# Kernel optimization log

Hardware: AMD Instinct MI355X
Metric: run time of the kernel (lower is better)

The kernel has to match this reference:

```python
import jax, jax.numpy as jnp
import numpy as np
from jax import lax

B, C, H, W, K = 64, 64, 128, 128, 4
EPS = 1e-5

def setup_inputs() -> dict:
    key = jax.random.key(0)
    ks = jax.random.split(key, 8)
    def p(i, shape, scale=0.05):
        return jax.random.normal(ks[i], shape, dtype=jnp.float32) * scale
    return {
        "rgb":   jax.random.normal(ks[0], (B, C, H, W), dtype=jnp.float32),
        "depth": jax.random.normal(ks[1], (B, C, H, W), dtype=jnp.float32),
        # kernel_gen MLP: Linear(2C->C), Linear(C -> K*C*9)
        "w1": p(2, (C, 2 * C)), "b1": jnp.zeros((C,), jnp.float32),
        "w2": p(3, (K * C * 9, C)), "b2": jnp.zeros((K * C * 9,), jnp.float32),
        # freq_decompose: Conv3x3(C->C) + BN (eval-mode stats)
        "fd_w": p(4, (C, C, 3, 3)), "fd_b": jnp.zeros((C,), jnp.float32),
        "fd_scale": jnp.ones((C,), jnp.float32), "fd_bias": jnp.zeros((C,), jnp.float32),
        "fd_mean": jnp.zeros((C,), jnp.float32), "fd_var": jnp.ones((C,), jnp.float32),
        # fusion: Conv1x1(2C->C) + BN
        "fu_w": p(5, (C, 2 * C, 1, 1)), "fu_b": jnp.zeros((C,), jnp.float32),
        "fu_scale": jnp.ones((C,), jnp.float32), "fu_bias": jnp.zeros((C,), jnp.float32),
        "fu_mean": jnp.zeros((C,), jnp.float32), "fu_var": jnp.ones((C,), jnp.float32),
    }

def _bn(x, scale, bias, mean, var):
    # eval-mode batchnorm over channel axis 1
    inv = scale / jnp.sqrt(var + EPS)
    return x * inv[None, :, None, None] + (bias - mean * inv)[None, :, None, None]

def _conv(x, w, pad):
    return lax.conv_general_dilated(x, w, (1, 1), ((pad, pad), (pad, pad)),
                                    dimension_numbers=("NCHW", "OIHW", "NCHW"))

def reference(rgb, depth, w1, b1, w2, b2,
              fd_w, fd_b, fd_scale, fd_bias, fd_mean, fd_var,
              fu_w, fu_b, fu_scale, fu_bias, fu_mean, fu_var):
    b, c, h, w = rgb.shape
    k = w2.shape[0] // (c * 9)
    # kernel generation: global avg pool over concat -> MLP
    pooled = jnp.concatenate([rgb, depth], axis=1).mean(axis=(2, 3))  # [B, 2C]
    hid = jax.nn.relu(pooled @ w1.T + b1)                             # [B, C]
    kernels = (hid @ w2.T + b2).reshape(b, k, c, 3, 3)                # [B, K, C, 3, 3]
    norms = jnp.linalg.norm(kernels.reshape(b, k, -1), axis=2)        # [B, K]
    attn = jax.nn.softmax(norms, axis=1)
    weighted_kernel = jnp.einsum("bk,bkcij->bcij", attn, kernels)     # [B, C, 3, 3]
    # NOTE: faithful to the torch code: plain conv2d with out_channels=B (requires B==C)
    dynamic_feat = _conv(rgb, weighted_kernel, 1)                     # [B, B, H, W]
    freq_feat = jax.nn.relu(_bn(_conv(depth, fd_w, 1) + fd_b[None, :, None, None],
                                fd_scale, fd_bias, fd_mean, fd_var))
    cat = jnp.concatenate([dynamic_feat, freq_feat], axis=1)          # [B, 2C, H, W]
    fused = jax.nn.relu(_bn(_conv(cat, fu_w, 0) + fu_b[None, :, None, None],
                            fu_scale, fu_bias, fu_mean, fu_var))
    return fused
```

## Files before the change

kernel.cpp:

```cpp
#include <hip/hip_runtime.h>
#include <hip/hip_bf16.h>

#define CB 64
#define HH 128
#define WW 128
#define KK 4
#define EPSV 1e-5f
#define HWSZ (HH*WW)

using f32x4   = __attribute__((ext_vector_type(4))) float;
using f32x16  = __attribute__((ext_vector_type(16))) float;
using short8  = __attribute__((ext_vector_type(8))) short;

static constexpr size_t WS_POOLED = 0;
static constexpr size_t WS_HID    = 8192;
static constexpr size_t WS_KERN   = 12288;
static constexpr size_t WS_SSQ    = 159744;
static constexpr size_t WS_WK     = 160000;
static constexpr size_t WS_EFFW   = 196864;
static constexpr size_t WS_FUW2   = 233728;
static constexpr size_t WS_FDINV  = 237824;
static constexpr size_t WS_FDBETA = 237888;
static constexpr size_t WS_FUINV  = 237952;
static constexpr size_t WS_FUBETA = 238016;
static constexpr size_t WT3_BYTE = 49152;
static constexpr size_t WFD_BYTE = 49152 + 73728;
static constexpr size_t W1_BYTE  = 49152 + 147456;
static constexpr size_t WS_PART_BYTE   = 4u << 20;
static constexpr size_t WS_DEPTHT_BYTE = 8u << 20;
static constexpr size_t WS_RGBT_BYTE   = 140u << 20;


__global__ void k_consts(const float* __restrict__ fd_scale, const float* __restrict__ fd_bias,
                         const float* __restrict__ fd_mean, const float* __restrict__ fd_var,
                         const float* __restrict__ fd_b,
                         const float* __restrict__ fu_scale, const float* __restrict__ fu_bias,
                         const float* __restrict__ fu_mean, const float* __restrict__ fu_var,
                         const float* __restrict__ fu_b,
                         float* __restrict__ ws) {
    int c = threadIdx.x;
    if (c < CB) {
        float fdi = fd_scale[c] / sqrtf(fd_var[c] + EPSV);
        ws[WS_FDINV + c]  = fdi;
        ws[WS_FDBETA + c] = (fd_b[c] - fd_mean[c]) * fdi + fd_bias[c];
        float fui = fu_scale[c] / sqrtf(fu_var[c] + EPSV);
        ws[WS_FUINV + c]  = fui;
        ws[WS_FUBETA + c] = (fu_b[c] - fu_mean[c]) * fui + fu_bias[c];
    }
}

__device__ __forceinline__ unsigned int pack_bf16(float a, float b) {
    __hip_bfloat16 ha = __float2bfloat16(a), hb = __float2bfloat16(b);
    return (unsigned int)*(unsigned short*)&ha | ((unsigned int)*(unsigned short*)&hb << 16);
}

__global__ __launch_bounds__(256) void k_nhwc(const float* __restrict__ rgb,
                                              const float* __restrict__ depth,
                                              unsigned int* __restrict__ rgbT,
                                              unsigned int* __restrict__ depthT,
                                              float* __restrict__ part) {
    int g = blockIdx.x;
    int b = blockIdx.y;
    int t = threadIdx.x;

    if (g == 64) {
        unsigned int* dR0 = rgbT   + ((size_t)b * 130 + 0)   * 130 * 32;
        unsigned int* dR1 = rgbT   + ((size_t)b * 130 + 129) * 130 * 32;
        unsigned int* dD0 = depthT + ((size_t)b * 130 + 0)   * 130 * 32;
        unsigned int* dD1 = depthT + ((size_t)b * 130 + 129) * 130 * 32;
        for (int i = t; i < 130 * 32; i += 256) {
            dR0[i] = 0u; dR1[i] = 0u; dD0[i] = 0u; dD1[i] = 0u;
        }
        return;
    }
    int y0 = g * 2;
    {
        int tensor = t >> 7, side = (t >> 6) & 1, row = (t >> 5) & 1, j = t & 31;
        unsigned int* d = tensor ? depthT : rgbT;
        d[(((size_t)b * 130 + (y0 + 1 + row)) * 130 + (side ? 129 : 0)) * 32 + j] = 0u;
    }

    __shared__ float staged[32][260];
    __shared__ float poolacc[128];
    int w = t >> 6, lane = t & 63;

    #pragma unroll
    for (int ph = 0; ph < 4; ++ph) {
        const float* src = (ph >> 1) ? depth : rgb;
        int chbase = (ph & 1) * 32;
        if (ph) __syncthreads();
        #pragma unroll
        for (int i = 0; i < 8; ++i) {
            int flat = i * 256 + t;
            int c = flat >> 6, f4 = flat & 63;
            const float4* sp = (const float4*)(src + ((size_t)(b * CB + chbase + c)) * HWSZ
                                               + (size_t)y0 * WW);
            float4 v = sp[f4];
            *(float4*)&staged[c][f4 * 4] = v;
            float s = v.x + v.y + v.z + v.w;
            #pragma unroll
            for (int off = 32; off; off >>= 1) s += __shfl_down(s, off, 64);
            if (lane == 0) poolacc[(ph >> 1) * 64 + chbase + i * 4 + w] = s;
        }
        __syncthreads();
        {
            int row = t >> 7, x = t & 127;
            unsigned int u[16];
            #pragma unroll
            for (int k = 0; k < 16; ++k)
                u[k] = pack_bf16(staged[2 * k][t], staged[2 * k + 1][t]);
            unsigned int* dst = (ph >> 1) ? depthT : rgbT;
            unsigned int* dp = dst + (((size_t)b * 130 + (y0 + 1 + row)) * 130 + 1 + x) * 32
                                   + (chbase >> 1);
            *(uint4*)dp        = *(uint4*)&u[0];
            *(uint4*)(dp + 4)  = *(uint4*)&u[4];
            *(uint4*)(dp + 8)  = *(uint4*)&u[8];
            *(uint4*)(dp + 12) = *(uint4*)&u[12];
        }
    }
    __syncthreads();
    if (t < 128)
        part[((size_t)b * 64 + g) * 128 + t] = poolacc[t];
}

__global__ __launch_bounds__(256) void k_pool2(const float* __restrict__ part,
                                               float* __restrict__ ws) {
    int b = blockIdx.x, t = threadIdx.x, cc = t & 127, q = t >> 7;
    float s = 0.f;
    for (int g = q * 32; g < q * 32 + 32; ++g)
        s += part[((size_t)b * 64 + g) * 128 + cc];
    __shared__ float red[2][128];
    red[q][cc] = s;
    __syncthreads();
    if (t < 128)
        ws[WS_POOLED + b * 128 + t] = (red[0][t] + red[1][t]) * (1.f / 16384.f);
}

__global__ void k_hid(const float* __restrict__ w1, const float* __restrict__ b1,
                      float* __restrict__ ws) {
    __shared__ float p[128];
    int b = blockIdx.x, j = threadIdx.x;
    p[j] = ws[WS_POOLED + b * 128 + j];
    __syncthreads();
    if (j < CB) {
        float s = b1[j];
        const float* wr = w1 + j * 128;
        #pragma unroll 8
        for (int i = 0; i < 128; ++i) s += p[i] * wr[i];
        ws[WS_HID + b * CB + j] = fmaxf(s, 0.f);
    }
}

__global__ __launch_bounds__(256) void k_kern(const float* __restrict__ w2, const float* __restrict__ b2,
                                              float* __restrict__ ws) {
    __shared__ float h[CB];
    int b = blockIdx.x, t = threadIdx.x;
    if (t < CB) h[t] = ws[WS_HID + b * CB + t];
    __syncthreads();
    float local = 0.f;
    #pragma unroll
    for (int r9 = 0; r9 < 9; ++r9) {
        int r = t * 9 + r9;
        float s = b2[r];
        const float* wr = w2 + r * CB;
        #pragma unroll 8
        for (int m = 0; m < CB; ++m) s += h[m] * wr[m];
        ws[WS_KERN + b * 2304 + r] = s;
        local += s * s;
    }
    #pragma unroll
    for (int off = 32; off; off >>= 1) local += __shfl_down(local, off, 64);
    if ((t & 63) == 0) ws[WS_SSQ + b * KK + (t >> 6)] = local;
}

__global__ __launch_bounds__(256) void k_wk(float* __restrict__ ws) {
    __shared__ float attn[KK];
    int b = blockIdx.x, t = threadIdx.x;
    if (t == 0) {
        float n[KK], m = -1e30f;
        #pragma unroll
        for (int k = 0; k < KK; ++k) { n[k] = sqrtf(ws[WS_SSQ + b * KK + k]); m = fmaxf(m, n[k]); }
        float e[KK], den = 0.f;
        #pragma unroll
        for (int k = 0; k < KK; ++k) { e[k] = expf(n[k] - m); den += e[k]; }
        float inv = 1.f / den;
        #pragma unroll
        for (int k = 0; k < KK; ++k) attn[k] = e[k] * inv;
    }
    __syncthreads();
    const float* kb = ws + WS_KERN + b * 2304;
    float a0 = attn[0], a1 = attn[1], a2 = attn[2], a3 = attn[3];
    for (int idx = t; idx < 576; idx += 256) {
        float s = a0 * kb[idx] + a1 * kb[576 + idx] + a2 * kb[1152 + idx] + a3 * kb[1728 + idx];
        ws[WS_WK + b * 576 + idx] = s;
    }
}

__global__ __launch_bounds__(256) void k_effw(const float* __restrict__ fu_w, float* __restrict__ ws) {
    int o = blockIdx.x, t = threadIdx.x;
    __shared__ float fw[CB];
    float fi = ws[WS_FUINV + o];
    if (t < CB) {
        fw[t] = fu_w[o * 128 + t] * fi;
        ws[WS_FUW2 + o * CB + t] = fu_w[o * 128 + CB + t] * fi;
    }
    __syncthreads();
    for (int idx = t; idx < 576; idx += 256) {
        float s = 0.f;
        #pragma unroll 8
        for (int c = 0; c < CB; ++c) s += fw[c] * ws[WS_WK + c * 576 + idx];
        ws[WS_EFFW + o * 576 + idx] = s;
    }
}

__global__ void k_prepw(const float* __restrict__ fd_w, float* __restrict__ ws) {
    int e = blockIdx.x * 256 + threadIdx.x;
    unsigned short* wt3 = (unsigned short*)((char*)ws + WT3_BYTE);
    unsigned short* wfd = (unsigned short*)((char*)ws + WFD_BYTE);
    unsigned short* w1o = (unsigned short*)((char*)ws + W1_BYTE);
    if (e < 73728) {
        int set = (e >= 36864) ? 1 : 0;
        int e2 = set ? e - 36864 : e;
        int j = e2 & 7, l = (e2 >> 3) & 63, oh = (e2 >> 9) & 1, Kq = (e2 >> 10) & 3, tap = e2 >> 12;
        int och = oh * 32 + (l & 31);
        int cin = Kq * 16 + (l >> 5) * 8 + j;
        float v = set ? fd_w[(och * 64 + cin) * 9 + tap] * ws[WS_FDINV + och]
                      : ws[WS_EFFW + och * 576 + cin * 9 + tap];
        __hip_bfloat16 h = __float2bfloat16(v);
        (set ? wfd : wt3)[e2] = *(unsigned short*)&h;
    } else if (e < 77824) {
        int e3 = e - 73728;
        int j = e3 & 7, l = (e3 >> 3) & 63, oh = (e3 >> 9) & 1, Kq = e3 >> 10;
        int och = oh * 32 + (l & 31);
        int cin = Kq * 16 + (l >> 5) * 8 + j;
        __hip_bfloat16 h = __float2bfloat16(ws[WS_FUW2 + och * CB + cin]);
        w1o[e3] = *(unsigned short*)&h;
    }
}


__device__ __forceinline__ void gload_lds16(const void* g, void* l) {
    __builtin_amdgcn_global_load_lds((const __attribute__((address_space(1))) unsigned int*)g,
                                     (__attribute__((address_space(3))) unsigned int*)l, 16, 0, 0);
}

__device__ __forceinline__ void stage_async(const unsigned short* __restrict__ T, int b,
                                            int y0p, int x0p, int t, char* tile) {
    const char* base = (const char*)(T + (((size_t)b * 130 + y0p) * 130 + x0p) * 64);
    #pragma unroll
    for (int it = 0; it < 10; ++it) {
        int n = it * 256 + t;
        int row = n / 272, rem = n - row * 272;
        int xx = rem >> 3, cs = rem & 7;
        gload_lds16(base + (size_t)row * 16640 + xx * 128 + ((cs ^ (xx & 7)) << 4),
                    tile + n * 16);
    }
    if (t < 160) {
        int n = 2560 + t;
        int row = n / 272, rem = n - row * 272;
        int xx = rem >> 3, cs = rem & 7;
        gload_lds16(base + (size_t)row * 16640 + xx * 128 + ((cs ^ (xx & 7)) << 4),
                    tile + n * 16);
    }
}

__device__ __forceinline__ void conv3x3w2(f32x16 (&acc)[2][2], const unsigned short* __restrict__ Wt,
                                          const char* tile, int w, int lane) {
    int px = lane & 31, hi = lane >> 5;
    #pragma unroll
    for (int tap = 0; tap < 9; ++tap) {
        const int di = tap / 3, dj = tap % 3;
        short8 wa[2][4];
        #pragma unroll
        for (int Kq = 0; Kq < 4; ++Kq)
            #pragma unroll
            for (int oh = 0; oh < 2; ++oh)
                wa[oh][Kq] = *(const short8*)(Wt + ((((tap * 4 + Kq) * 2 + oh) * 64 + lane) << 3));
        const int xx = px + dj;
        #pragma unroll
        for (int pxg = 0; pxg < 2; ++pxg) {
            const char* base = tile + (w * 2 + pxg + di) * 4352 + xx * 128;
            #pragma unroll
            for (int Kq = 0; Kq < 4; ++Kq) {
                short8 bf = *(const short8*)(base + (((Kq * 2 + hi) ^ (xx & 7)) << 4));
                __builtin_amdgcn_s_setprio(1);
                acc[0][pxg] = __builtin_amdgcn_mfma_f32_32x32x16_bf16(wa[0][Kq], bf, acc[0][pxg], 0, 0, 0);
                acc[1][pxg] = __builtin_amdgcn_mfma_f32_32x32x16_bf16(wa[1][Kq], bf, acc[1][pxg], 0, 0, 0);
                __builtin_amdgcn_s_setprio(0);
            }
        }
    }
}

__global__ __launch_bounds__(256, 2) void k_fused(const unsigned short* __restrict__ rgbT,
                                                  const unsigned short* __restrict__ depthT,
                                                  const float* __restrict__ ws,
                                                  float* __restrict__ out) {
    __shared__ __align__(16) char tile[43520];
    int b = blockIdx.z;
    int x0 = blockIdx.x * 32, y0 = blockIdx.y * 8;
    int t = threadIdx.x, lane = t & 63, w = t >> 6;
    int px = lane & 31, hi = lane >> 5;

    const unsigned short* wfd = (const unsigned short*)((const char*)ws + WFD_BYTE);
    const unsigned short* wt3 = (const unsigned short*)((const char*)ws + WT3_BYTE);
    const unsigned short* w1o = (const unsigned short*)((const char*)ws + W1_BYTE);

    stage_async(depthT, b, y0, x0, t, tile);

    f32x16 facc[2][2];
    #pragma unroll
    for (int oh = 0; oh < 2; ++oh) {
        f32x16 bi;
        #pragma unroll
        for (int r = 0; r < 16; ++r)
            bi[r] = ws[WS_FDBETA + oh * 32 + (r & 3) + 8 * (r >> 2) + 4 * hi];
        facc[oh][0] = bi;
        facc[oh][1] = bi;
    }
    __syncthreads();

    conv3x3w2(facc, wfd, tile, w, lane);
    __syncthreads();

    {
        unsigned int* fl = (unsigned int*)tile;
        #pragma unroll
        for (int oh = 0; oh < 2; ++oh)
            #pragma unroll
            for (int pxg = 0; pxg < 2; ++pxg) {
                int p = (w * 2 + pxg) * 32 + px;
                #pragma unroll
                for (int q = 0; q < 4; ++q) {
                    unsigned int u0 = pack_bf16(fmaxf(facc[oh][pxg][q * 4 + 0], 0.f),
                                                fmaxf(facc[oh][pxg][q * 4 + 1], 0.f));
                    unsigned int u1 = pack_bf16(fmaxf(facc[oh][pxg][q * 4 + 2], 0.f),
                                                fmaxf(facc[oh][pxg][q * 4 + 3], 0.f));
                    int slot = (q + oh * 4) ^ (p & 7);
                    int dw = p * 32 + slot * 4 + hi * 2;
                    fl[dw] = u0;
                    fl[dw + 1] = u1;
                }
            }
    }
    __syncthreads();

    f32x16 acc[2][2];
    #pragma unroll
    for (int oh = 0; oh < 2; ++oh) {
        f32x16 bi;
        #pragma unroll
        for (int r = 0; r < 16; ++r)
            bi[r] = ws[WS_FUBETA + oh * 32 + (r & 3) + 8 * (r >> 2) + 4 * hi];
        acc[oh][0] = bi;
        acc[oh][1] = bi;
    }
    #pragma unroll
    for (int Kq = 0; Kq < 4; ++Kq) {
        short8 w1a[2];
        #pragma unroll
        for (int oh = 0; oh < 2; ++oh)
            w1a[oh] = *(const short8*)(w1o + (((Kq * 2 + oh) * 64 + lane) << 3));
        #pragma unroll
        for (int pxg = 0; pxg < 2; ++pxg) {
            int p = (w * 2 + pxg) * 32 + px;
            short8 bf = *(const short8*)(tile + p * 128 + (((Kq * 2 + hi) ^ (p & 7)) << 4));
            __builtin_amdgcn_s_setprio(1);
            acc[0][pxg] = __builtin_amdgcn_mfma_f32_32x32x16_bf16(w1a[0], bf, acc[0][pxg], 0, 0, 0);
            acc[1][pxg] = __builtin_amdgcn_mfma_f32_32x32x16_bf16(w1a[1], bf, acc[1][pxg], 0, 0, 0);
            __builtin_amdgcn_s_setprio(0);
        }
    }
    __syncthreads();

    stage_async(rgbT, b, y0, x0, t, tile);
    __syncthreads();

    conv3x3w2(acc, wt3, tile, w, lane);
    __syncthreads();

    float* slab = (float*)(tile + w * 8704);
    #pragma unroll
    for (int pxg = 0; pxg < 2; ++pxg) {
        #pragma unroll
        for (int oh = 0; oh < 2; ++oh)
            #pragma unroll
            for (int q = 0; q < 4; ++q)
                #pragma unroll
                for (int i = 0; i < 4; ++i)
                    slab[(oh * 32 + q * 8 + hi * 4 + i) * 33 + px] =
                        fmaxf(acc[oh][pxg][q * 4 + i], 0.f);
        int y = y0 + w * 2 + pxg;
        #pragma unroll
        for (int c2 = 0; c2 < 32; ++c2) {
            int c = c2 * 2 + hi;
            out[(size_t)(b * CB + c) * HWSZ + (size_t)y * WW + x0 + px] = slab[c * 33 + px];
        }
    }
}


extern "C" void kernel_launch(void* const* d_in, const int* in_sizes, int n_in,
                              void* d_out, int out_size, void* d_ws, size_t ws_size,
                              hipStream_t stream) {
    const float* rgb      = (const float*)d_in[0];
    const float* depth    = (const float*)d_in[1];
    const float* w1       = (const float*)d_in[2];
    const float* b1       = (const float*)d_in[3];
    const float* w2       = (const float*)d_in[4];
    const float* b2       = (const float*)d_in[5];
    const float* fd_w     = (const float*)d_in[6];
    const float* fd_b     = (const float*)d_in[7];
    const float* fd_scale = (const float*)d_in[8];
    const float* fd_bias  = (const float*)d_in[9];
    const float* fd_mean  = (const float*)d_in[10];
    const float* fd_var   = (const float*)d_in[11];
    const float* fu_w     = (const float*)d_in[12];
    const float* fu_b     = (const float*)d_in[13];
    const float* fu_scale = (const float*)d_in[14];
    const float* fu_bias  = (const float*)d_in[15];
    const float* fu_mean  = (const float*)d_in[16];
    const float* fu_var   = (const float*)d_in[17];

    float* ws = (float*)d_ws;
    float* part = (float*)((char*)d_ws + WS_PART_BYTE);
    unsigned int* depthT = (unsigned int*)((char*)d_ws + WS_DEPTHT_BYTE);
    unsigned int* rgbT   = (unsigned int*)((char*)d_ws + WS_RGBT_BYTE);
    float* out = (float*)d_out;

    k_consts<<<1, 64, 0, stream>>>(fd_scale, fd_bias, fd_mean, fd_var, fd_b,
                                   fu_scale, fu_bias, fu_mean, fu_var, fu_b, ws);
    k_nhwc<<<dim3(65, 64), 256, 0, stream>>>(rgb, depth, rgbT, depthT, part);
    k_pool2<<<CB, 256, 0, stream>>>(part, ws);
    k_hid<<<CB, 128, 0, stream>>>(w1, b1, ws);
    k_kern<<<CB, 256, 0, stream>>>(w2, b2, ws);
    k_wk<<<CB, 256, 0, stream>>>(ws);
    k_effw<<<CB, 256, 0, stream>>>(fu_w, ws);
    k_prepw<<<304, 256, 0, stream>>>(fd_w, ws);

    dim3 grid(WW / 32, HH / 8, CB);
    k_fused<<<grid, 256, 0, stream>>>((const unsigned short*)rgbT,
                                      (const unsigned short*)depthT, ws, out);
}
```

Before: 473.2 us.

## Overlap rgb tile staging with 1x1 fusion and split 3x3 conv by channel halves

The input tile is now staged as channel-slab-major planes in two halves. A partial vmcnt wait lets the first half of the 3x3 conv start while the second half of the load is still in flight. The 1x1 fusion intermediate moves to a separate LDS buffer, so the rgb tile load can be issued right after the depth conv and overlap the fusion MFMAs. LDS per block grows to about 76 KB, which still allows two blocks per CU, at the cost of fragile hand-coded waitcnt logic.

```diff
diff --git a/kernel.cpp b/kernel.cpp
--- a/kernel.cpp
+++ b/kernel.cpp
@@ -244,48 +244,57 @@
                                      (__attribute__((address_space(3))) unsigned int*)l, 16, 0, 0);
 }
 
-__device__ __forceinline__ void stage_async(const unsigned short* __restrict__ T, int b,
-                                            int y0p, int x0p, int t, char* tile) {
+__device__ __forceinline__ void stage12(const unsigned short* __restrict__ T, int b,
+                                        int y0p, int x0p, int t, char* tile) {
     const char* base = (const char*)(T + (((size_t)b * 130 + y0p) * 130 + x0p) * 64);
     #pragma unroll
-    for (int it = 0; it < 10; ++it) {
-        int n = it * 256 + t;
-        int row = n / 272, rem = n - row * 272;
-        int xx = rem >> 3, cs = rem & 7;
-        gload_lds16(base + (size_t)row * 16640 + xx * 128 + ((cs ^ (xx & 7)) << 4),
-                    tile + n * 16);
-    }
-    if (t < 160) {
-        int n = 2560 + t;
-        int row = n / 272, rem = n - row * 272;
-        int xx = rem >> 3, cs = rem & 7;
-        gload_lds16(base + (size_t)row * 16640 + xx * 128 + ((cs ^ (xx & 7)) << 4),
-                    tile + n * 16);
-    }
-}
-
-__device__ __forceinline__ void conv3x3w2(f32x16 (&acc)[2][2], const unsigned short* __restrict__ Wt,
-                                          const char* tile, int w, int lane) {
+    for (int h = 0; h < 2; ++h) {
+        #pragma unroll
+        for (int k = 0; k < 5; ++k) {
+            int m = h * 1360 + k * 256 + t;
+            int cs = m / 340, pix = m - cs * 340;
+            int row = pix / 34, xx = pix - row * 34;
+            gload_lds16(base + (size_t)row * 16640 + xx * 128 + cs * 16, tile + m * 16);
+        }
+        if (t < 80) {
+            int m = h * 1360 + 1280 + t;
+            int cs = m / 340, pix = m - cs * 340;
+            int row = pix / 34, xx = pix - row * 34;
+            gload_lds16(base + (size_t)row * 16640 + xx * 128 + cs * 16, tile + m * 16);
+        }
+    }
+}
+
+#define WAIT_HALF1() do {                                   \
+    asm volatile("s_waitcnt vmcnt(5)" ::: "memory");        \
+    __builtin_amdgcn_s_barrier();                           \
+    __builtin_amdgcn_sched_barrier(0);                      \
+} while (0)
+
+template<int KQ0>
+__device__ __forceinline__ void convH(f32x16 (&acc)[2][2], const unsigned short* __restrict__ Wt,
+                                      const char* tile, int w, int lane) {
     int px = lane & 31, hi = lane >> 5;
     #pragma unroll
     for (int tap = 0; tap < 9; ++tap) {
         const int di = tap / 3, dj = tap % 3;
-        short8 wa[2][4];
-        #pragma unroll
-        for (int Kq = 0; Kq < 4; ++Kq)
+        const int xx = px + dj;
+        short8 wa[2][2];
+        #pragma unroll
+        for (int k = 0; k < 2; ++k)
             #pragma unroll
             for (int oh = 0; oh < 2; ++oh)
-                wa[oh][Kq] = *(const short8*)(Wt + ((((tap * 4 + Kq) * 2 + oh) * 64 + lane) << 3));
-        const int xx = px + dj;
-        #pragma unroll
-        for (int pxg = 0; pxg < 2; ++pxg) {
-            const char* base = tile + (w * 2 + pxg + di) * 4352 + xx * 128;
-            #pragma unroll
-            for (int Kq = 0; Kq < 4; ++Kq) {
-                short8 bf = *(const short8*)(base + (((Kq * 2 + hi) ^ (xx & 7)) << 4));
+                wa[k][oh] = *(const short8*)(Wt + ((((tap * 4 + KQ0 + k) * 2 + oh) * 64 + lane) << 3));
+        #pragma unroll
+        for (int k = 0; k < 2; ++k) {
+            #pragma unroll
+            for (int pxg = 0; pxg < 2; ++pxg) {
+                int row = w * 2 + pxg + di;
+                short8 bf = *(const short8*)(tile + (size_t)((KQ0 + k) * 2 + hi) * 5440
+                                             + (row * 34 + xx) * 16);
                 __builtin_amdgcn_s_setprio(1);
-                acc[0][pxg] = __builtin_amdgcn_mfma_f32_32x32x16_bf16(wa[0][Kq], bf, acc[0][pxg], 0, 0, 0);
-                acc[1][pxg] = __builtin_amdgcn_mfma_f32_32x32x16_bf16(wa[1][Kq], bf, acc[1][pxg], 0, 0, 0);
+                acc[0][pxg] = __builtin_amdgcn_mfma_f32_32x32x16_bf16(wa[k][0], bf, acc[0][pxg], 0, 0, 0);
+                acc[1][pxg] = __builtin_amdgcn_mfma_f32_32x32x16_bf16(wa[k][1], bf, acc[1][pxg], 0, 0, 0);
                 __builtin_amdgcn_s_setprio(0);
             }
         }
@@ -296,7 +305,8 @@
                                                   const unsigned short* __restrict__ depthT,
                                                   const float* __restrict__ ws,
                                                   float* __restrict__ out) {
-    __shared__ __align__(16) char tile[43520];
+    __shared__ __align__(16) char tile[76288];
+    char* T2 = tile + 43520;
     int b = blockIdx.z;
     int x0 = blockIdx.x * 32, y0 = blockIdx.y * 8;
     int t = threadIdx.x, lane = t & 63, w = t >> 6;
@@ -306,7 +316,9 @@
     const unsigned short* wt3 = (const unsigned short*)((const char*)ws + WT3_BYTE);
     const unsigned short* w1o = (const unsigned short*)((const char*)ws + W1_BYTE);
 
-    stage_async(depthT, b, y0, x0, t, tile);
+    stage12(depthT, b, y0, x0, t, tile);
+
+    WAIT_HALF1();
 
     f32x16 facc[2][2];
     #pragma unroll
@@ -318,32 +330,29 @@
         facc[oh][0] = bi;
         facc[oh][1] = bi;
     }
-    __syncthreads();
-
-    conv3x3w2(facc, wfd, tile, w, lane);
-    __syncthreads();
-
-    {
-        unsigned int* fl = (unsigned int*)tile;
-        #pragma unroll
-        for (int oh = 0; oh < 2; ++oh)
-            #pragma unroll
-            for (int pxg = 0; pxg < 2; ++pxg) {
-                int p = (w * 2 + pxg) * 32 + px;
-                #pragma unroll
-                for (int q = 0; q < 4; ++q) {
-                    unsigned int u0 = pack_bf16(fmaxf(facc[oh][pxg][q * 4 + 0], 0.f),
-                                                fmaxf(facc[oh][pxg][q * 4 + 1], 0.f));
-                    unsigned int u1 = pack_bf16(fmaxf(facc[oh][pxg][q * 4 + 2], 0.f),
-                                                fmaxf(facc[oh][pxg][q * 4 + 3], 0.f));
-                    int slot = (q + oh * 4) ^ (p & 7);
-                    int dw = p * 32 + slot * 4 + hi * 2;
-                    fl[dw] = u0;
-                    fl[dw + 1] = u1;
-                }
+
+    convH<0>(facc, wfd, tile, w, lane);
+    __syncthreads();
+    convH<2>(facc, wfd, tile, w, lane);
+    __syncthreads();
+
+    stage12(rgbT, b, y0, x0, t, tile);
+
+    #pragma unroll
+    for (int oh = 0; oh < 2; ++oh)
+        #pragma unroll
+        for (int pxg = 0; pxg < 2; ++pxg) {
+            int p = (w * 2 + pxg) * 32 + px;
+            #pragma unroll
+            for (int q = 0; q < 4; ++q) {
+                unsigned int u0 = pack_bf16(fmaxf(facc[oh][pxg][q * 4 + 0], 0.f),
+                                            fmaxf(facc[oh][pxg][q * 4 + 1], 0.f));
+                unsigned int u1 = pack_bf16(fmaxf(facc[oh][pxg][q * 4 + 2], 0.f),
+                                            fmaxf(facc[oh][pxg][q * 4 + 3], 0.f));
+                uint2 uu = {u0, u1};
+                *(uint2*)(T2 + (size_t)(oh * 4 + q) * 4096 + p * 16 + hi * 8) = uu;
             }
-    }
-    __syncthreads();
+        }
 
     f32x16 acc[2][2];
     #pragma unroll
@@ -364,19 +373,19 @@
         #pragma unroll
         for (int pxg = 0; pxg < 2; ++pxg) {
             int p = (w * 2 + pxg) * 32 + px;
-            short8 bf = *(const short8*)(tile + p * 128 + (((Kq * 2 + hi) ^ (p & 7)) << 4));
+            short8 bf = *(const short8*)(T2 + (size_t)(Kq * 2 + hi) * 4096 + p * 16);
             __builtin_amdgcn_s_setprio(1);
             acc[0][pxg] = __builtin_amdgcn_mfma_f32_32x32x16_bf16(w1a[0], bf, acc[0][pxg], 0, 0, 0);
             acc[1][pxg] = __builtin_amdgcn_mfma_f32_32x32x16_bf16(w1a[1], bf, acc[1][pxg], 0, 0, 0);
             __builtin_amdgcn_s_setprio(0);
         }
     }
-    __syncthreads();
-
-    stage_async(rgbT, b, y0, x0, t, tile);
-    __syncthreads();
-
-    conv3x3w2(acc, wt3, tile, w, lane);
+
+    WAIT_HALF1();
+
+    convH<0>(acc, wt3, tile, w, lane);
+    __syncthreads();
+    convH<2>(acc, wt3, tile, w, lane);
     __syncthreads();
 
     float* slab = (float*)(tile + w * 8704);
```

Result: slower. 508.0 us (+7.4%).

## Pack bf16 pairs at load time in transpose kernel and raise fused kernel occupancy

Applied to the files above, without the earlier changes.

The transpose/pool kernel now loads two channels per wavefront, packs them into bf16 pairs before writing to shared memory, and processes all 64 channels of a tensor in one phase instead of two. This halves the shared staging traffic and cuts the number of phases and barriers. The fused conv kernel's launch bounds are raised to request three blocks per SM, and its accumulator array is reused across both convolutions to reduce register pressure. Forcing the higher occupancy may cause register spills. LDS use (about 43.5KB per block) could still limit residency.

```diff
diff --git a/kernel.cpp b/kernel.cpp
--- a/kernel.cpp
+++ b/kernel.cpp
@@ -80,42 +80,55 @@
         d[(((size_t)b * 130 + (y0 + 1 + row)) * 130 + (side ? 129 : 0)) * 32 + j] = 0u;
     }
 
-    __shared__ float staged[32][260];
+    __shared__ unsigned int staged[32][260];
     __shared__ float poolacc[128];
     int w = t >> 6, lane = t & 63;
 
     #pragma unroll
-    for (int ph = 0; ph < 4; ++ph) {
-        const float* src = (ph >> 1) ? depth : rgb;
-        int chbase = (ph & 1) * 32;
+    for (int ph = 0; ph < 2; ++ph) {
+        const float* src = ph ? depth : rgb;
+        unsigned int* dst = ph ? depthT : rgbT;
         if (ph) __syncthreads();
+
         #pragma unroll
         for (int i = 0; i < 8; ++i) {
-            int flat = i * 256 + t;
-            int c = flat >> 6, f4 = flat & 63;
-            const float4* sp = (const float4*)(src + ((size_t)(b * CB + chbase + c)) * HWSZ
+            int pair = i * 4 + w;
+            int c = pair * 2;
+            const float4* s0 = (const float4*)(src + ((size_t)(b * CB + c)) * HWSZ
                                                + (size_t)y0 * WW);
-            float4 v = sp[f4];
-            *(float4*)&staged[c][f4 * 4] = v;
-            float s = v.x + v.y + v.z + v.w;
-            #pragma unroll
-            for (int off = 32; off; off >>= 1) s += __shfl_down(s, off, 64);
-            if (lane == 0) poolacc[(ph >> 1) * 64 + chbase + i * 4 + w] = s;
+            const float4* s1 = (const float4*)(src + ((size_t)(b * CB + c + 1)) * HWSZ
+                                               + (size_t)y0 * WW);
+            float4 v0 = s0[lane];
+            float4 v1 = s1[lane];
+            unsigned int pk0 = pack_bf16(v0.x, v1.x);
+            unsigned int pk1 = pack_bf16(v0.y, v1.y);
+            unsigned int pk2 = pack_bf16(v0.z, v1.z);
+            unsigned int pk3 = pack_bf16(v0.w, v1.w);
+            uint4 q = {pk0, pk1, pk2, pk3};
+            *(uint4*)&staged[pair][lane * 4] = q;
+            float sa = v0.x + v0.y + v0.z + v0.w;
+            float sb = v1.x + v1.y + v1.z + v1.w;
+            #pragma unroll
+            for (int off = 32; off; off >>= 1) {
+                sa += __shfl_down(sa, off, 64);
+                sb += __shfl_down(sb, off, 64);
+            }
+            if (lane == 0) {
+                poolacc[ph * 64 + c]     = sa;
+                poolacc[ph * 64 + c + 1] = sb;
+            }
         }
         __syncthreads();
+
         {
             int row = t >> 7, x = t & 127;
-            unsigned int u[16];
-            #pragma unroll
-            for (int k = 0; k < 16; ++k)
-                u[k] = pack_bf16(staged[2 * k][t], staged[2 * k + 1][t]);
-            unsigned int* dst = (ph >> 1) ? depthT : rgbT;
-            unsigned int* dp = dst + (((size_t)b * 130 + (y0 + 1 + row)) * 130 + 1 + x) * 32
-                                   + (chbase >> 1);
-            *(uint4*)dp        = *(uint4*)&u[0];
-            *(uint4*)(dp + 4)  = *(uint4*)&u[4];
-            *(uint4*)(dp + 8)  = *(uint4*)&u[8];
-            *(uint4*)(dp + 12) = *(uint4*)&u[12];
+            unsigned int line[32];
+            #pragma unroll
+            for (int p = 0; p < 32; ++p) line[p] = staged[p][t];
+            unsigned int* dp = dst + (((size_t)b * 130 + (y0 + 1 + row)) * 130 + 1 + x) * 32;
+            #pragma unroll
+            for (int q = 0; q < 8; ++q)
+                *(uint4*)(dp + q * 4) = *(uint4*)&line[q * 4];
         }
     }
     __syncthreads();
@@ -292,7 +305,7 @@
     }
 }
 
-__global__ __launch_bounds__(256, 2) void k_fused(const unsigned short* __restrict__ rgbT,
+__global__ __launch_bounds__(256, 3) void k_fused(const unsigned short* __restrict__ rgbT,
                                                   const unsigned short* __restrict__ depthT,
                                                   const float* __restrict__ ws,
                                                   float* __restrict__ out) {
@@ -308,19 +321,19 @@
 
     stage_async(depthT, b, y0, x0, t, tile);
 
-    f32x16 facc[2][2];
+    f32x16 acc[2][2];
     #pragma unroll
     for (int oh = 0; oh < 2; ++oh) {
         f32x16 bi;
         #pragma unroll
         for (int r = 0; r < 16; ++r)
             bi[r] = ws[WS_FDBETA + oh * 32 + (r & 3) + 8 * (r >> 2) + 4 * hi];
-        facc[oh][0] = bi;
-        facc[oh][1] = bi;
-    }
-    __syncthreads();
-
-    conv3x3w2(facc, wfd, tile, w, lane);
+        acc[oh][0] = bi;
+        acc[oh][1] = bi;
+    }
+    __syncthreads();
+
+    conv3x3w2(acc, wfd, tile, w, lane);
     __syncthreads();
 
     {
@@ -332,10 +345,10 @@
                 int p = (w * 2 + pxg) * 32 + px;
                 #pragma unroll
                 for (int q = 0; q < 4; ++q) {
-                    unsigned int u0 = pack_bf16(fmaxf(facc[oh][pxg][q * 4 + 0], 0.f),
-                                                fmaxf(facc[oh][pxg][q * 4 + 1], 0.f));
-                    unsigned int u1 = pack_bf16(fmaxf(facc[oh][pxg][q * 4 + 2], 0.f),
-                                                fmaxf(facc[oh][pxg][q * 4 + 3], 0.f));
+                    unsigned int u0 = pack_bf16(fmaxf(acc[oh][pxg][q * 4 + 0], 0.f),
+                                                fmaxf(acc[oh][pxg][q * 4 + 1], 0.f));
+                    unsigned int u1 = pack_bf16(fmaxf(acc[oh][pxg][q * 4 + 2], 0.f),
+                                                fmaxf(acc[oh][pxg][q * 4 + 3], 0.f));
                     int slot = (q + oh * 4) ^ (p & 7);
                     int dw = p * 32 + slot * 4 + hi * 2;
                     fl[dw] = u0;
@@ -345,7 +358,6 @@
     }
     __syncthreads();
 
-    f32x16 acc[2][2];
     #pragma unroll
     for (int oh = 0; oh < 2; ++oh) {
         f32x16 bi;
```

New measurement: 477.5 us. Within noise of the previous version (+0.9%).
